# Optimization experiments

Measured on AMD Instinct MI355X. Metric: run time of the kernel, lower is better.

## Reference

```python
import jax, jax.numpy as jnp
import numpy as np

EPS = 1e-5

def _bn(x, g, b):
    # BatchNorm1d in training mode: batch statistics over nodes
    m = jnp.mean(x, axis=0)
    v = jnp.var(x, axis=0)
    return g * (x - m) * jax.lax.rsqrt(v + EPS) + b

def _gconv(x, adj, W, b):
    # GraphConvolution: adj @ x @ W + b
    return adj @ (x @ W) + b

def _gsage(x, adj, W, b):
    # GraphSAGE layer: relu(adj @ x @ W + b)
    return jax.nn.relu(adj @ (x @ W) + b)

def setup_inputs() -> dict:
    key = jax.random.key(0)
    ks = jax.random.split(key, 20)
    N = 8192
    x = jax.random.normal(ks[0], (N, 18), dtype=jnp.float32)
    adj = jax.random.uniform(ks[1], (N, N), dtype=jnp.float32)
    s = 0.1
    p = {
        'W1': jax.random.normal(ks[2], (18, 16)) * s, 'b1': jnp.zeros((16,)),
        'W2': jax.random.normal(ks[3], (16, 16)) * s, 'b2': jnp.zeros((16,)),
        'We1': jax.random.normal(ks[4], (16, 8)) * s, 'be1': jnp.zeros((8,)),
        'Wp1': jax.random.normal(ks[5], (16, 20)) * s, 'bp1': jnp.zeros((20,)),
        'W3': jax.random.normal(ks[6], (8, 8)) * s, 'b3': jnp.zeros((8,)),
        'We2': jax.random.normal(ks[7], (8, 8)) * s, 'be2': jnp.zeros((8,)),
        'g1': jnp.ones((16,)), 'bt1': jnp.zeros((16,)),
        'g2': jnp.ones((16,)), 'bt2': jnp.zeros((16,)),
        'g3': jnp.ones((8,)), 'bt3': jnp.zeros((8,)),
    }
    p = {k: v.astype(jnp.float32) for k, v in p.items()}
    return {'x': x, 'adj': adj, **p}

def reference(x, adj, W1, b1, W2, b2, We1, be1, Wp1, bp1, W3, b3, We2, be2,
              g1, bt1, g2, bt2, g3, bt3):
    h = _bn(_gsage(x, adj, W1, b1), g1, bt1)          # [N,16]
    h = _bn(_gsage(h, adj, W2, b2), g2, bt2)          # [N,16]
    # DiffPool(16, 20, 8)
    z = _gconv(h, adj, We1, be1)                      # [N,8]
    s_l = jax.nn.softmax(_gconv(h, adj, Wp1, bp1), axis=1)  # [N,20]
    h = s_l.T @ z                                     # [20,8]
    a = s_l.T @ adj @ s_l                             # [20,20]
    h = _bn(_gsage(h, a, W3, b3), g3, bt3)            # [20,8]
    # DiffPool(8, 1, 8, is_final=True): s = ones -> column sum
    z = _gconv(h, a, We2, be2)                        # [20,8]
    return jnp.sum(z, axis=0, keepdims=True)          # [1,8]
```

## Files before the change

### kernel.cpp

```cpp
#include <hip/hip_runtime.h>
#include <cstddef>

#define NROWS 8192
constexpr float BN_EPS = 1e-5f;

typedef __attribute__((ext_vector_type(8))) short bf16x8;
typedef __attribute__((ext_vector_type(4))) float f32x4;
typedef __attribute__((ext_vector_type(2))) float f32x2;
typedef __attribute__((ext_vector_type(4))) unsigned int u32x4;

__device__ __forceinline__ unsigned short bf16u(float f) {
    unsigned u = __float_as_uint(f);
    u += 0x7FFFu + ((u >> 16) & 1u);
    return (unsigned short)(u >> 16);
}
__device__ __forceinline__ unsigned bf16pk(float x, float y) {
    return (unsigned)bf16u(x) | ((unsigned)bf16u(y) << 16);
}

constexpr size_t OFF_P   = 0;
constexpr size_t OFF_YP  = OFF_P   + (size_t)16 * NROWS * 32;
constexpr size_t OFF_SLP = OFF_YP  + (size_t)NROWS * 32 / 2;
constexpr size_t OFF_U   = OFF_SLP + (size_t)NROWS * 32 / 2;
constexpr size_t OFF_SL  = OFF_U   + (size_t)NROWS * 16;
constexpr size_t OFF_ST1 = OFF_SL  + (size_t)NROWS * 20;
constexpr size_t OFF_ST2 = OFF_ST1 + 32;
constexpr size_t OFF_HSM = OFF_ST2 + 32;
constexpr size_t OFF_AG  = OFF_HSM + 160;
constexpr size_t OFF_CTR = OFF_AG  + 400;
constexpr int    NSMALL  = 32 + 32 + 160 + 400 + 2;
constexpr size_t OFF_END_SMALL = OFF_CTR + 2;
constexpr size_t OFF_ADJB = (OFF_END_SMALL + 15) & ~(size_t)15;
constexpr size_t NEED_FULL_BYTES = (OFF_ADJB + (size_t)NROWS * NROWS / 2) * 4;


__global__ __launch_bounds__(256)
void k_conv_spmm(const float* __restrict__ adjf, unsigned short* __restrict__ adjp,
                 const unsigned short* __restrict__ ypu, float* __restrict__ P)
{
    __shared__ unsigned short lds[16384];
    const int bid = blockIdx.x;
    const int rb = bid & 63, kc = bid >> 6;
    const int t = threadIdx.x, lane = t & 63, wv = t >> 6;
    const int row0 = rb * 128 + wv * 32;
    const int s_q = lane >> 4;
    const int khi = (lane >> 2) & 3;
    const int el2 = (lane & 3) * 2;
    const bf16x8* ap = (const bf16x8*)lds;
    const bf16x8* yp = (const bf16x8*)ypu;
    const size_t blockbase = (size_t)(kc * 64 + rb) * 8192;

    f32x4 acc0 = (f32x4){0.f,0.f,0.f,0.f}, acc1 = (f32x4){0.f,0.f,0.f,0.f};

    for (int q = 0; q < 4; ++q) {
        const int kbase = kc * 512 + q * 128;
        __syncthreads();
#pragma unroll 8
        for (int rr = 0; rr < 32; ++rr) {
            const f32x2 v = *(const f32x2*)(adjf + (size_t)(row0 + rr) * NROWS + kbase + lane * 2);
            const int m = rr >> 4, rA = rr & 15;
            int u = ((wv * 4 + s_q) * 2 + m) * 64 + rA + 16 * khi;
            u ^= ((u >> 4) & 3) ^ (((u >> 7) & 1) << 2);
            *(unsigned*)&lds[u * 8 + el2] = bf16pk(v.x, v.y);
        }
        __syncthreads();
#pragma unroll
        for (int i = 0; i < 8; ++i) {
            const int flat = i * 256 + t;
            const int phys = flat ^ ((flat >> 4) & 3) ^ (((flat >> 7) & 1) << 2);
            const u32x4 d = *(const u32x4*)&lds[phys * 8];
            const int wvd = flat >> 9;
            const size_t gu = blockbase + (size_t)wvd * 2048 + (size_t)q * 512 + (flat & 511);
            *(u32x4*)(adjp + gu * 8) = d;
        }
#pragma unroll
        for (int sq = 0; sq < 4; ++sq) {
            int L0 = ((wv * 4 + sq) * 2 + 0) * 64 + lane;
            int L1 = L0 + 64;
            L0 ^= ((L0 >> 4) & 3) ^ (((L0 >> 7) & 1) << 2);
            L1 ^= ((L1 >> 4) & 3) ^ (((L1 >> 7) & 1) << 2);
            const bf16x8 a0 = ap[L0];
            const bf16x8 a1 = ap[L1];
            const bf16x8 b0 = yp[((size_t)(kc * 16 + q * 4 + sq)) * 64 + lane];
            acc0 = __builtin_amdgcn_mfma_f32_16x16x32_bf16(a0, b0, acc0, 0, 0, 0);
            acc1 = __builtin_amdgcn_mfma_f32_16x16x32_bf16(a1, b0, acc1, 0, 0, 0);
        }
    }

    float* Pk = P + ((size_t)kc * NROWS + row0) * 16;
    const int drow = (lane >> 4) * 4;
    const int dcol = lane & 15;
#pragma unroll
    for (int r = 0; r < 4; ++r) {
        Pk[(size_t)(drow + r) * 16 + dcol]      = acc0[r];
        Pk[(size_t)(16 + drow + r) * 16 + dcol] = acc1[r];
    }
}

template<int NT, int CO>
__global__ __launch_bounds__(256)
void k_spmm_p(const unsigned short* __restrict__ adjp,
              const unsigned short* __restrict__ ypu, float* __restrict__ P)
{
    constexpr int CP = NT * 16;
    const int rb   = blockIdx.x & 63;
    const int kc2  = blockIdx.x >> 6;
    const int lane = threadIdx.x & 63;
    const int wv   = threadIdx.x >> 6;
    const int row0 = rb * 128 + wv * 32;
    const bf16x8* ap = (const bf16x8*)adjp;
    const bf16x8* yp = (const bf16x8*)ypu;
    const size_t wbase0 = ((size_t)((kc2 * 2 + 0) * 64 + rb) * 4 + wv) * 2048;
    const size_t wbase1 = ((size_t)((kc2 * 2 + 1) * 64 + rb) * 4 + wv) * 2048;

    f32x4 acc[2][NT];
#pragma unroll
    for (int m = 0; m < 2; ++m)
#pragma unroll
        for (int n = 0; n < NT; ++n) acc[m][n] = (f32x4){0.f, 0.f, 0.f, 0.f};

    auto LA = [&](int m, int s) -> bf16x8 {
        const size_t wb = (s < 16) ? wbase0 : wbase1;
        return ap[wb + (size_t)(s & 15) * 128 + m * 64 + lane];
    };
    auto LB = [&](int n, int s) -> bf16x8 {
        return yp[((size_t)((kc2 * 32 + s) * NT + n)) * 64 + lane];
    };

    bf16x8 a0 = LA(0, 0), a1 = LA(1, 0);
    bf16x8 b0 = LB(0, 0), b1;
    if constexpr (NT == 2) b1 = LB(1, 0);

#pragma unroll
    for (int s = 0; s < 32; ++s) {
        bf16x8 na0, na1, nb0, nb1;
        if (s < 31) {
            na0 = LA(0, s + 1); na1 = LA(1, s + 1);
            nb0 = LB(0, s + 1);
            if constexpr (NT == 2) nb1 = LB(1, s + 1);
        }
        acc[0][0] = __builtin_amdgcn_mfma_f32_16x16x32_bf16(a0, b0, acc[0][0], 0, 0, 0);
        acc[1][0] = __builtin_amdgcn_mfma_f32_16x16x32_bf16(a1, b0, acc[1][0], 0, 0, 0);
        if constexpr (NT == 2) {
            acc[0][1] = __builtin_amdgcn_mfma_f32_16x16x32_bf16(a0, b1, acc[0][1], 0, 0, 0);
            acc[1][1] = __builtin_amdgcn_mfma_f32_16x16x32_bf16(a1, b1, acc[1][1], 0, 0, 0);
        }
        if (s < 31) { a0 = na0; a1 = na1; b0 = nb0; if constexpr (NT == 2) b1 = nb1; }
    }

    float* Pk = P + ((size_t)kc2 * NROWS + row0) * CP;
    const int drow = (lane >> 4) * 4;
    const int dcol = lane & 15;
#pragma unroll
    for (int m = 0; m < 2; ++m)
#pragma unroll
        for (int n = 0; n < NT; ++n)
            if (n * 16 + 0 < CO)
#pragma unroll
                for (int r = 0; r < 4; ++r)
                    if (n * 16 + dcol < CO)
                        Pk[(size_t)(m * 16 + drow + r) * CP + n * 16 + dcol] = acc[m][n][r];
}

template<int NT, int CO>
__global__ __launch_bounds__(256)
void k_spmm_f32(const float* __restrict__ adjf,
                const unsigned short* __restrict__ ypu, float* __restrict__ P)
{
    constexpr int CP = NT * 16;
    const int rb   = blockIdx.x & 63;
    const int kc   = blockIdx.x >> 6;
    const int lane = threadIdx.x & 63;
    const int wv   = threadIdx.x >> 6;
    const int row0 = rb * 128 + wv * 32;
    const int k0   = kc * 512;
    const int rA   = lane & 15;
    const int kA   = (lane >> 4) * 8;
    const bf16x8* yp = (const bf16x8*)ypu;

    f32x4 acc[2][NT];
#pragma unroll
    for (int m = 0; m < 2; ++m)
#pragma unroll
        for (int n = 0; n < NT; ++n) acc[m][n] = (f32x4){0.f, 0.f, 0.f, 0.f};

    const size_t offA0 = (size_t)(row0 + rA) * NROWS + k0 + kA;
    const size_t offA1 = offA0 + (size_t)16 * NROWS;

    auto LA = [&](int m, int s) -> bf16x8 {
        const size_t o = (m ? offA1 : offA0) + (size_t)s * 32;
        const f32x4 u = *(const f32x4*)(adjf + o);
        const f32x4 v = *(const f32x4*)(adjf + o + 4);
        bf16x8 tt;
        tt[0] = (short)bf16u(u.x); tt[1] = (short)bf16u(u.y);
        tt[2] = (short)bf16u(u.z); tt[3] = (short)bf16u(u.w);
        tt[4] = (short)bf16u(v.x); tt[5] = (short)bf16u(v.y);
        tt[6] = (short)bf16u(v.z); tt[7] = (short)bf16u(v.w);
        return tt;
    };
    auto LB = [&](int n, int s) -> bf16x8 {
        return yp[((size_t)((kc * 16 + s) * NT + n)) * 64 + lane];
    };

    bf16x8 a0 = LA(0, 0), a1 = LA(1, 0);
    bf16x8 b0 = LB(0, 0), b1;
    if constexpr (NT == 2) b1 = LB(1, 0);

#pragma unroll
    for (int s = 0; s < 16; ++s) {
        bf16x8 na0, na1, nb0, nb1;
        if (s < 15) {
            na0 = LA(0, s + 1); na1 = LA(1, s + 1);
            nb0 = LB(0, s + 1);
            if constexpr (NT == 2) nb1 = LB(1, s + 1);
        }
        acc[0][0] = __builtin_amdgcn_mfma_f32_16x16x32_bf16(a0, b0, acc[0][0], 0, 0, 0);
        acc[1][0] = __builtin_amdgcn_mfma_f32_16x16x32_bf16(a1, b0, acc[1][0], 0, 0, 0);
        if constexpr (NT == 2) {
            acc[0][1] = __builtin_amdgcn_mfma_f32_16x16x32_bf16(a0, b1, acc[0][1], 0, 0, 0);
            acc[1][1] = __builtin_amdgcn_mfma_f32_16x16x32_bf16(a1, b1, acc[1][1], 0, 0, 0);
        }
        if (s < 15) { a0 = na0; a1 = na1; b0 = nb0; if constexpr (NT == 2) b1 = nb1; }
    }

    float* Pk = P + ((size_t)kc * NROWS + row0) * CP;
    const int drow = (lane >> 4) * 4;
    const int dcol = lane & 15;
#pragma unroll
    for (int m = 0; m < 2; ++m)
#pragma unroll
        for (int n = 0; n < NT; ++n)
            if (n * 16 + 0 < CO)
#pragma unroll
                for (int r = 0; r < 4; ++r)
                    if (n * 16 + dcol < CO)
                        Pk[(size_t)(m * 16 + drow + r) * CP + n * 16 + dcol] = acc[m][n][r];
}

__global__ __launch_bounds__(256)
void k_y1_pack(const float* __restrict__ x, const float* __restrict__ W1,
               unsigned short* __restrict__ yp, float* __restrict__ zsmall)
{
    if (blockIdx.x == 0) {
        for (int i = threadIdx.x; i < NSMALL; i += 256) zsmall[i] = 0.f;
    }
    const int j = blockIdx.x * 256 + threadIdx.x;
    float xr[18];
#pragma unroll
    for (int d = 0; d < 18; ++d) xr[d] = x[j * 18 + d];
    const int kb = j >> 5, lhi = ((j & 31) >> 3) << 4, idx = j & 7;
#pragma unroll
    for (int c = 0; c < 16; ++c) {
        float a = 0.f;
#pragma unroll
        for (int d = 0; d < 18; ++d) a = fmaf(xr[d], W1[d * 16 + c], a);
        yp[((size_t)kb * 64 + (lhi | c)) * 8 + idx] = bf16u(a);
    }
}

template<int KCN, int COA, int COB, int NTO>
__global__ __launch_bounds__(256)
void k_red_bn(const float* __restrict__ P, const float* __restrict__ bias,
              const float* __restrict__ g, const float* __restrict__ bt,
              const float* __restrict__ Wa, const float* __restrict__ Wb,
              unsigned short* __restrict__ yp, float* __restrict__ stats,
              unsigned int* __restrict__ ctr)
{
    const int t = threadIdx.x, col = t & 15, rg = t >> 4;
    const int rbase = blockIdx.x * 128;
    float u[8];
    float s = 0.f, ss = 0.f;
#pragma unroll
    for (int i = 0; i < 8; ++i) {
        const int r = rbase + rg + i * 16;
        float v = bias[col];
#pragma unroll
        for (int kc = 0; kc < KCN; ++kc)
            v += P[((size_t)kc * NROWS + r) * 16 + col];
        v = fmaxf(v, 0.f);
        u[i] = v; s += v; ss += v * v;
    }
    __shared__ float ls[16][17], lss[16][17];
    __shared__ float hb[128][17];
    __shared__ float scb[16], shb[16];
    ls[rg][col] = s; lss[rg][col] = ss;
    __syncthreads();
    if (t < 16) {
        float a = 0.f, b = 0.f;
        for (int gg = 0; gg < 16; ++gg) { a += ls[gg][t]; b += lss[gg][t]; }
        atomicAdd(&stats[t], a);
        atomicAdd(&stats[16 + t], b);
    }
    __syncthreads();
    if (t == 0) {
        __threadfence();
        atomicAdd(ctr, 1u);
        while (__hip_atomic_load(ctr, __ATOMIC_RELAXED, __HIP_MEMORY_SCOPE_AGENT) < 64u) {}
        __threadfence();
    }
    __syncthreads();
    if (t < 16) {
        const float sm  = atomicAdd(&stats[t], 0.f);
        const float sq  = atomicAdd(&stats[16 + t], 0.f);
        const float m   = sm * (1.f / NROWS);
        const float var = sq * (1.f / NROWS) - m * m;
        const float sc  = g[t] * rsqrtf(var + BN_EPS);
        scb[t] = sc; shb[t] = bt[t] - m * sc;
    }
    __syncthreads();
#pragma unroll
    for (int i = 0; i < 8; ++i)
        hb[rg + i * 16][col] = fmaf(u[i], scb[col], shb[col]);
    __syncthreads();
    constexpr int CO = COA + COB;
    const int lrow = t >> 1;
    const int jrow = rbase + lrow;
    const int kb = jrow >> 5, lhi = ((jrow & 31) >> 3) << 4, idx = jrow & 7;
    auto slot = [&](int c) -> size_t {
        return ((size_t)(kb * NTO + (c >> 4)) * 64 + (lhi | (c & 15))) * 8 + idx;
    };
    float h[16];
#pragma unroll
    for (int k = 0; k < 16; ++k) h[k] = hb[lrow][k];
    const int c0 = (t & 1) * ((NTO * 16) / 2);
#pragma unroll
    for (int cc = 0; cc < (NTO * 16) / 2; ++cc) {
        const int c = c0 + cc;
        float a = 0.f;
        if (c < COA) {
#pragma unroll
            for (int k = 0; k < 16; ++k) a = fmaf(h[k], Wa[k * COA + c], a);
        } else if (c < CO) {
#pragma unroll
            for (int k = 0; k < 16; ++k) a = fmaf(h[k], Wb[k * COB + (c - COA)], a);
        }
        yp[slot(c)] = (c < CO) ? bf16u(a) : (unsigned short)0;
    }
}

template<int KCN>
__global__ __launch_bounds__(256)
void k_red_fin3(const float* __restrict__ P, const float* __restrict__ be1,
                const float* __restrict__ bp1, float* __restrict__ sl,
                unsigned short* __restrict__ slp, float* __restrict__ hsm)
{
    __shared__ float szl[256 * 8];
    __shared__ float ssl[256 * 20];
    const int t = threadIdx.x;
    const int row = blockIdx.x * 256 + t;

    float s3[28];
#pragma unroll
    for (int c = 0; c < 28; ++c) s3[c] = 0.f;
#pragma unroll
    for (int kc = 0; kc < KCN; ++kc) {
        const float* pr = &P[((size_t)kc * NROWS + row) * 32];
#pragma unroll
        for (int q = 0; q < 7; ++q) {
            const f32x4 v = *(const f32x4*)(pr + q * 4);
            s3[q * 4 + 0] += v.x; s3[q * 4 + 1] += v.y;
            s3[q * 4 + 2] += v.z; s3[q * 4 + 3] += v.w;
        }
    }
#pragma unroll
    for (int k = 0; k < 8; ++k) szl[t * 8 + k] = s3[k] + be1[k];

    float s[20];
    float mx = -1e30f;
#pragma unroll
    for (int k = 0; k < 20; ++k) {
        s[k] = s3[8 + k] + bp1[k];
        mx = fmaxf(mx, s[k]);
    }
    float se = 0.f;
#pragma unroll
    for (int k = 0; k < 20; ++k) { s[k] = expf(s[k] - mx); se += s[k]; }
    const float inv = 1.f / se;
    const int kb = row >> 5, lhi = ((row & 31) >> 3) << 4, idx = row & 7;
    auto slot = [&](int c) -> size_t {
        return ((size_t)(kb * 2 + (c >> 4)) * 64 + (lhi | (c & 15))) * 8 + idx;
    };
#pragma unroll
    for (int k = 0; k < 20; ++k) {
        s[k] *= inv;
        sl[(size_t)row * 20 + k] = s[k];
        ssl[t * 20 + k] = s[k];
        slp[slot(k)] = bf16u(s[k]);
    }
#pragma unroll
    for (int c = 20; c < 32; ++c) slp[slot(c)] = 0;
    __syncthreads();
    if (t < 160) {
        const int p = t >> 3, q = t & 7;
        float a = 0.f;
        for (int r = 0; r < 256; ++r) a = fmaf(ssl[r * 20 + p], szl[r * 8 + q], a);
        atomicAdd(&hsm[t], a);
    }
}

template<int KCN>
__global__ __launch_bounds__(256)
void k_red_fin4(const float* __restrict__ P, const float* __restrict__ sl,
                float* __restrict__ a_g)
{
    __shared__ float stt[256 * 20];
    __shared__ float ssl[256 * 20];
    const int t = threadIdx.x;
    const int row = blockIdx.x * 256 + t;

    float t4[20];
#pragma unroll
    for (int c = 0; c < 20; ++c) t4[c] = 0.f;
#pragma unroll
    for (int kc = 0; kc < KCN; ++kc) {
        const float* pr = &P[((size_t)kc * NROWS + row) * 32];
#pragma unroll
        for (int q = 0; q < 5; ++q) {
            const f32x4 v = *(const f32x4*)(pr + q * 4);
            t4[q * 4 + 0] += v.x; t4[q * 4 + 1] += v.y;
            t4[q * 4 + 2] += v.z; t4[q * 4 + 3] += v.w;
        }
    }
#pragma unroll
    for (int c = 0; c < 20; ++c) {
        stt[t * 20 + c] = t4[c];
        ssl[t * 20 + c] = sl[(size_t)row * 20 + c];
    }
    __syncthreads();
    for (int pair = t; pair < 400; pair += 256) {
        const int p = pair / 20, q = pair % 20;
        float a = 0.f;
        for (int r = 0; r < 256; ++r) a = fmaf(ssl[r * 20 + p], stt[r * 20 + q], a);
        atomicAdd(&a_g[pair], a);
    }
}

__global__ __launch_bounds__(256)
void k_final(const float* __restrict__ hsm, const float* __restrict__ a_g,
             const float* __restrict__ W3, const float* __restrict__ b3,
             const float* __restrict__ g3, const float* __restrict__ bt3,
             const float* __restrict__ We2, const float* __restrict__ be2,
             float* __restrict__ out)
{
    __shared__ float m1[160], qb[160], hb[160], sc[8], sh[8];
    const int t = threadIdx.x;
    const int p = t >> 3, k = t & 7;
    if (t < 160) {
        float a = 0.f;
        for (int j = 0; j < 8; ++j) a = fmaf(hsm[p * 8 + j], W3[j * 8 + k], a);
        m1[t] = a;
    }
    __syncthreads();
    if (t < 160) {
        float a = b3[k];
        for (int j = 0; j < 20; ++j) a = fmaf(a_g[p * 20 + j], m1[j * 8 + k], a);
        qb[t] = fmaxf(a, 0.f);
    }
    __syncthreads();
    if (t < 8) {
        float m = 0.f, v = 0.f;
        for (int r = 0; r < 20; ++r) { float q = qb[r * 8 + t]; m += q; v += q * q; }
        m *= (1.f / 20.f); v = v * (1.f / 20.f) - m * m;
        const float s = g3[t] * rsqrtf(v + BN_EPS);
        sc[t] = s; sh[t] = bt3[t] - m * s;
    }
    __syncthreads();
    if (t < 160) hb[t] = fmaf(qb[t], sc[k], sh[k]);
    __syncthreads();
    if (t < 160) {
        float a = 0.f;
        for (int j = 0; j < 8; ++j) a = fmaf(hb[p * 8 + j], We2[j * 8 + k], a);
        m1[t] = a;
    }
    __syncthreads();
    if (t < 160) {
        float a = be2[k];
        for (int j = 0; j < 20; ++j) a = fmaf(a_g[p * 20 + j], m1[j * 8 + k], a);
        qb[t] = a;
    }
    __syncthreads();
    if (t < 8) {
        float a = 0.f;
        for (int r = 0; r < 20; ++r) a += qb[r * 8 + t];
        out[t] = a;
    }
}

extern "C" void kernel_launch(void* const* d_in, const int* in_sizes, int n_in,
                              void* d_out, int out_size, void* d_ws, size_t ws_size,
                              hipStream_t stream)
{
    const float* x   = (const float*)d_in[0];
    const float* adj = (const float*)d_in[1];
    const float* W1  = (const float*)d_in[2];
    const float* b1  = (const float*)d_in[3];
    const float* W2  = (const float*)d_in[4];
    const float* b2  = (const float*)d_in[5];
    const float* We1 = (const float*)d_in[6];
    const float* be1 = (const float*)d_in[7];
    const float* Wp1 = (const float*)d_in[8];
    const float* bp1 = (const float*)d_in[9];
    const float* W3  = (const float*)d_in[10];
    const float* b3  = (const float*)d_in[11];
    const float* We2 = (const float*)d_in[12];
    const float* be2 = (const float*)d_in[13];
    const float* g1  = (const float*)d_in[14];
    const float* bt1 = (const float*)d_in[15];
    const float* g2  = (const float*)d_in[16];
    const float* bt2 = (const float*)d_in[17];
    const float* g3  = (const float*)d_in[18];
    const float* bt3 = (const float*)d_in[19];

    float* ws = (float*)d_ws;
    float* P  = ws + OFF_P;
    unsigned short* YP   = (unsigned short*)(ws + OFF_YP);
    unsigned short* SLP  = (unsigned short*)(ws + OFF_SLP);
    float* SL  = ws + OFF_SL;
    float* ST1 = ws + OFF_ST1;
    float* ST2 = ws + OFF_ST2;
    float* HSM = ws + OFF_HSM;
    float* AG  = ws + OFF_AG;
    unsigned int* CTR = (unsigned int*)(ws + OFF_CTR);
    unsigned short* ADJP = (unsigned short*)(ws + OFF_ADJB);
    float* out = (float*)d_out;

    const bool FULL = ws_size >= NEED_FULL_BYTES;
    const dim3 blk(256);

    k_y1_pack<<<32, blk, 0, stream>>>(x, W1, YP, ST1);
    if (FULL) {
        k_conv_spmm<<<1024, blk, 0, stream>>>(adj, ADJP, YP, P);
        k_red_bn<16, 16, 0, 1><<<64, blk, 0, stream>>>(P, b1, g1, bt1, W2, nullptr, YP, ST1, CTR);

        k_spmm_p<1, 16><<<512, blk, 0, stream>>>(ADJP, YP, P);
        k_red_bn<8, 8, 20, 2><<<64, blk, 0, stream>>>(P, b2, g2, bt2, We1, Wp1, YP, ST2, CTR + 1);

        k_spmm_p<2, 28><<<512, blk, 0, stream>>>(ADJP, YP, P);
        k_red_fin3<8><<<32, blk, 0, stream>>>(P, be1, bp1, SL, SLP, HSM);

        k_spmm_p<2, 20><<<512, blk, 0, stream>>>(ADJP, SLP, P);
        k_red_fin4<8><<<32, blk, 0, stream>>>(P, SL, AG);
    } else {
        k_spmm_f32<1, 16><<<1024, blk, 0, stream>>>(adj, YP, P);
        k_red_bn<16, 16, 0, 1><<<64, blk, 0, stream>>>(P, b1, g1, bt1, W2, nullptr, YP, ST1, CTR);

        k_spmm_f32<1, 16><<<1024, blk, 0, stream>>>(adj, YP, P);
        k_red_bn<16, 8, 20, 2><<<64, blk, 0, stream>>>(P, b2, g2, bt2, We1, Wp1, YP, ST2, CTR + 1);

        k_spmm_f32<2, 28><<<1024, blk, 0, stream>>>(adj, YP, P);
        k_red_fin3<16><<<32, blk, 0, stream>>>(P, be1, bp1, SL, SLP, HSM);

        k_spmm_f32<2, 20><<<1024, blk, 0, stream>>>(adj, SLP, P);
        k_red_fin4<16><<<32, blk, 0, stream>>>(P, SL, AG);
    }

    k_final<<<1, blk, 0, stream>>>(HSM, AG, W3, b3, g3, bt3, We2, be2, out);
}
```

Before: 197.8 us.

## Fuse SpMM passes with their reductions using last-block grid sync

Merges each bf16 SpMM pass over the packed adjacency with the reduction/BN/softmax kernel that followed it. Every block bumps an atomic counter after writing partials, and the first 32 or 64 blocks spin until all 512 have arrived before doing the reduction. This removes three kernel launches and the gaps between them. In exchange the spinning blocks hold resources and rely on every block being co-resident or already finished, which risks deadlock. The change also adds launch-bounds occupancy hints and a larger unroll in the conversion kernel.

```diff
diff --git a/kernel.cpp b/kernel.cpp
--- a/kernel.cpp
+++ b/kernel.cpp
@@ -28,13 +28,13 @@
 constexpr size_t OFF_HSM = OFF_ST2 + 32;
 constexpr size_t OFF_AG  = OFF_HSM + 160;
 constexpr size_t OFF_CTR = OFF_AG  + 400;
-constexpr int    NSMALL  = 32 + 32 + 160 + 400 + 2;
-constexpr size_t OFF_END_SMALL = OFF_CTR + 2;
+constexpr int    NSMALL  = 32 + 32 + 160 + 400 + 8;
+constexpr size_t OFF_END_SMALL = OFF_CTR + 8;
 constexpr size_t OFF_ADJB = (OFF_END_SMALL + 15) & ~(size_t)15;
 constexpr size_t NEED_FULL_BYTES = (OFF_ADJB + (size_t)NROWS * NROWS / 2) * 4;
 
 
-__global__ __launch_bounds__(256)
+__global__ __launch_bounds__(256, 4)
 void k_conv_spmm(const float* __restrict__ adjf, unsigned short* __restrict__ adjp,
                  const unsigned short* __restrict__ ypu, float* __restrict__ P)
 {
@@ -55,7 +55,7 @@
     for (int q = 0; q < 4; ++q) {
         const int kbase = kc * 512 + q * 128;
         __syncthreads();
-#pragma unroll 8
+#pragma unroll 16
         for (int rr = 0; rr < 32; ++rr) {
             const f32x2 v = *(const f32x2*)(adjf + (size_t)(row0 + rr) * NROWS + kbase + lane * 2);
             const int m = rr >> 4, rA = rr & 15;
@@ -97,12 +97,137 @@
     }
 }
 
-template<int NT, int CO>
-__global__ __launch_bounds__(256)
-void k_spmm_p(const unsigned short* __restrict__ adjp,
-              const unsigned short* __restrict__ ypu, float* __restrict__ P)
-{
-    constexpr int CP = NT * 16;
+__global__ __launch_bounds__(256, 4)
+void k_spmm_bn(const unsigned short* __restrict__ adjp, unsigned short* yp_io,
+               float* __restrict__ P, const float* __restrict__ bias,
+               const float* __restrict__ g, const float* __restrict__ bt,
+               const float* __restrict__ Wa, const float* __restrict__ Wb,
+               float* __restrict__ stats, unsigned int* __restrict__ ctrs)
+{
+    const int rb   = blockIdx.x & 63;
+    const int kc2  = blockIdx.x >> 6;
+    const int lane = threadIdx.x & 63;
+    const int wv   = threadIdx.x >> 6;
+    const int row0 = rb * 128 + wv * 32;
+    const bf16x8* ap = (const bf16x8*)adjp;
+    const bf16x8* yp = (const bf16x8*)yp_io;
+    const size_t wbase0 = ((size_t)((kc2 * 2 + 0) * 64 + rb) * 4 + wv) * 2048;
+    const size_t wbase1 = ((size_t)((kc2 * 2 + 1) * 64 + rb) * 4 + wv) * 2048;
+
+    f32x4 acc0 = (f32x4){0.f,0.f,0.f,0.f}, acc1 = (f32x4){0.f,0.f,0.f,0.f};
+    auto LA = [&](int m, int s) -> bf16x8 {
+        const size_t wb = (s < 16) ? wbase0 : wbase1;
+        return ap[wb + (size_t)(s & 15) * 128 + m * 64 + lane];
+    };
+    auto LB = [&](int s) -> bf16x8 {
+        return yp[((size_t)(kc2 * 32 + s)) * 64 + lane];
+    };
+    bf16x8 a0 = LA(0, 0), a1 = LA(1, 0), b0 = LB(0);
+#pragma unroll
+    for (int s = 0; s < 32; ++s) {
+        bf16x8 na0, na1, nb0;
+        if (s < 31) { na0 = LA(0, s + 1); na1 = LA(1, s + 1); nb0 = LB(s + 1); }
+        acc0 = __builtin_amdgcn_mfma_f32_16x16x32_bf16(a0, b0, acc0, 0, 0, 0);
+        acc1 = __builtin_amdgcn_mfma_f32_16x16x32_bf16(a1, b0, acc1, 0, 0, 0);
+        if (s < 31) { a0 = na0; a1 = na1; b0 = nb0; }
+    }
+    {
+        float* Pk = P + ((size_t)kc2 * NROWS + row0) * 16;
+        const int drow = (lane >> 4) * 4, dcol = lane & 15;
+#pragma unroll
+        for (int r = 0; r < 4; ++r) {
+            Pk[(size_t)(drow + r) * 16 + dcol]      = acc0[r];
+            Pk[(size_t)(16 + drow + r) * 16 + dcol] = acc1[r];
+        }
+    }
+    __threadfence();
+    __syncthreads();
+    if (threadIdx.x == 0) atomicAdd(&ctrs[0], 1u);
+    if (blockIdx.x >= 64) return;
+    if (threadIdx.x == 0) {
+        while (__hip_atomic_load(&ctrs[0], __ATOMIC_RELAXED, __HIP_MEMORY_SCOPE_AGENT) < 512u) {}
+        __threadfence();
+    }
+    __syncthreads();
+
+    const int t = threadIdx.x, col = t & 15, rg = t >> 4;
+    const int rbase = blockIdx.x * 128;
+    float u[8];
+    float s = 0.f, ss = 0.f;
+#pragma unroll
+    for (int i = 0; i < 8; ++i) {
+        const int r = rbase + rg + i * 16;
+        float v = bias[col];
+#pragma unroll
+        for (int kc = 0; kc < 8; ++kc)
+            v += P[((size_t)kc * NROWS + r) * 16 + col];
+        v = fmaxf(v, 0.f);
+        u[i] = v; s += v; ss += v * v;
+    }
+    __shared__ float ls[16][17], lss[16][17];
+    __shared__ float hb[128][17];
+    __shared__ float scb[16], shb[16];
+    ls[rg][col] = s; lss[rg][col] = ss;
+    __syncthreads();
+    if (t < 16) {
+        float a = 0.f, b = 0.f;
+        for (int gg = 0; gg < 16; ++gg) { a += ls[gg][t]; b += lss[gg][t]; }
+        atomicAdd(&stats[t], a);
+        atomicAdd(&stats[16 + t], b);
+    }
+    __syncthreads();
+    if (t == 0) {
+        __threadfence();
+        atomicAdd(&ctrs[1], 1u);
+        while (__hip_atomic_load(&ctrs[1], __ATOMIC_RELAXED, __HIP_MEMORY_SCOPE_AGENT) < 64u) {}
+        __threadfence();
+    }
+    __syncthreads();
+    if (t < 16) {
+        const float sm  = atomicAdd(&stats[t], 0.f);
+        const float sq  = atomicAdd(&stats[16 + t], 0.f);
+        const float m   = sm * (1.f / NROWS);
+        const float var = sq * (1.f / NROWS) - m * m;
+        const float sc  = g[t] * rsqrtf(var + BN_EPS);
+        scb[t] = sc; shb[t] = bt[t] - m * sc;
+    }
+    __syncthreads();
+#pragma unroll
+    for (int i = 0; i < 8; ++i)
+        hb[rg + i * 16][col] = fmaf(u[i], scb[col], shb[col]);
+    __syncthreads();
+    const int lrow = t >> 1;
+    const int jrow = rbase + lrow;
+    const int kb = jrow >> 5, lhi = ((jrow & 31) >> 3) << 4, idx = jrow & 7;
+    auto slot = [&](int c) -> size_t {
+        return ((size_t)(kb * 2 + (c >> 4)) * 64 + (lhi | (c & 15))) * 8 + idx;
+    };
+    float h[16];
+#pragma unroll
+    for (int k = 0; k < 16; ++k) h[k] = hb[lrow][k];
+    const int c0 = (t & 1) * 16;
+#pragma unroll
+    for (int cc = 0; cc < 16; ++cc) {
+        const int c = c0 + cc;
+        float a = 0.f;
+        if (c < 8) {
+#pragma unroll
+            for (int k = 0; k < 16; ++k) a = fmaf(h[k], Wa[k * 8 + c], a);
+        } else if (c < 28) {
+#pragma unroll
+            for (int k = 0; k < 16; ++k) a = fmaf(h[k], Wb[k * 20 + (c - 8)], a);
+        }
+        yp_io[slot(c)] = (c < 28) ? bf16u(a) : (unsigned short)0;
+    }
+}
+
+__global__ __launch_bounds__(256, 4)
+void k_spmm_fin3(const unsigned short* __restrict__ adjp,
+                 const unsigned short* __restrict__ ypu, float* __restrict__ P,
+                 const float* __restrict__ be1, const float* __restrict__ bp1,
+                 float* __restrict__ sl, unsigned short* __restrict__ slp,
+                 float* __restrict__ hsm, unsigned int* __restrict__ ctr)
+{
     const int rb   = blockIdx.x & 63;
     const int kc2  = blockIdx.x >> 6;
     const int lane = threadIdx.x & 63;
@@ -113,53 +238,193 @@
     const size_t wbase0 = ((size_t)((kc2 * 2 + 0) * 64 + rb) * 4 + wv) * 2048;
     const size_t wbase1 = ((size_t)((kc2 * 2 + 1) * 64 + rb) * 4 + wv) * 2048;
 
-    f32x4 acc[2][NT];
+    f32x4 acc[2][2];
 #pragma unroll
     for (int m = 0; m < 2; ++m)
 #pragma unroll
-        for (int n = 0; n < NT; ++n) acc[m][n] = (f32x4){0.f, 0.f, 0.f, 0.f};
-
+        for (int n = 0; n < 2; ++n) acc[m][n] = (f32x4){0.f, 0.f, 0.f, 0.f};
     auto LA = [&](int m, int s) -> bf16x8 {
         const size_t wb = (s < 16) ? wbase0 : wbase1;
         return ap[wb + (size_t)(s & 15) * 128 + m * 64 + lane];
     };
     auto LB = [&](int n, int s) -> bf16x8 {
-        return yp[((size_t)((kc2 * 32 + s) * NT + n)) * 64 + lane];
-    };
-
-    bf16x8 a0 = LA(0, 0), a1 = LA(1, 0);
-    bf16x8 b0 = LB(0, 0), b1;
-    if constexpr (NT == 2) b1 = LB(1, 0);
-
+        return yp[((size_t)((kc2 * 32 + s) * 2 + n)) * 64 + lane];
+    };
+    bf16x8 a0 = LA(0, 0), a1 = LA(1, 0), b0 = LB(0, 0), b1 = LB(1, 0);
 #pragma unroll
     for (int s = 0; s < 32; ++s) {
         bf16x8 na0, na1, nb0, nb1;
-        if (s < 31) {
-            na0 = LA(0, s + 1); na1 = LA(1, s + 1);
-            nb0 = LB(0, s + 1);
-            if constexpr (NT == 2) nb1 = LB(1, s + 1);
-        }
+        if (s < 31) { na0 = LA(0, s+1); na1 = LA(1, s+1); nb0 = LB(0, s+1); nb1 = LB(1, s+1); }
         acc[0][0] = __builtin_amdgcn_mfma_f32_16x16x32_bf16(a0, b0, acc[0][0], 0, 0, 0);
         acc[1][0] = __builtin_amdgcn_mfma_f32_16x16x32_bf16(a1, b0, acc[1][0], 0, 0, 0);
-        if constexpr (NT == 2) {
-            acc[0][1] = __builtin_amdgcn_mfma_f32_16x16x32_bf16(a0, b1, acc[0][1], 0, 0, 0);
-            acc[1][1] = __builtin_amdgcn_mfma_f32_16x16x32_bf16(a1, b1, acc[1][1], 0, 0, 0);
-        }
-        if (s < 31) { a0 = na0; a1 = na1; b0 = nb0; if constexpr (NT == 2) b1 = nb1; }
-    }
-
-    float* Pk = P + ((size_t)kc2 * NROWS + row0) * CP;
-    const int drow = (lane >> 4) * 4;
-    const int dcol = lane & 15;
+        acc[0][1] = __builtin_amdgcn_mfma_f32_16x16x32_bf16(a0, b1, acc[0][1], 0, 0, 0);
+        acc[1][1] = __builtin_amdgcn_mfma_f32_16x16x32_bf16(a1, b1, acc[1][1], 0, 0, 0);
+        if (s < 31) { a0 = na0; a1 = na1; b0 = nb0; b1 = nb1; }
+    }
+    {
+        float* Pk = P + ((size_t)kc2 * NROWS + row0) * 32;
+        const int drow = (lane >> 4) * 4, dcol = lane & 15;
+#pragma unroll
+        for (int m = 0; m < 2; ++m)
+#pragma unroll
+            for (int n = 0; n < 2; ++n)
+#pragma unroll
+                for (int r = 0; r < 4; ++r)
+                    if (n * 16 + dcol < 28)
+                        Pk[(size_t)(m * 16 + drow + r) * 32 + n * 16 + dcol] = acc[m][n][r];
+    }
+    __threadfence();
+    __syncthreads();
+    if (threadIdx.x == 0) atomicAdd(ctr, 1u);
+    if (blockIdx.x >= 32) return;
+    if (threadIdx.x == 0) {
+        while (__hip_atomic_load(ctr, __ATOMIC_RELAXED, __HIP_MEMORY_SCOPE_AGENT) < 512u) {}
+        __threadfence();
+    }
+    __syncthreads();
+
+    __shared__ float szl[256 * 8];
+    __shared__ float ssl[256 * 20];
+    const int t = threadIdx.x;
+    const int row = blockIdx.x * 256 + t;
+    float s3[28];
+#pragma unroll
+    for (int c = 0; c < 28; ++c) s3[c] = 0.f;
+#pragma unroll
+    for (int kc = 0; kc < 8; ++kc) {
+        const float* pr = &P[((size_t)kc * NROWS + row) * 32];
+#pragma unroll
+        for (int q = 0; q < 7; ++q) {
+            const f32x4 v = *(const f32x4*)(pr + q * 4);
+            s3[q * 4 + 0] += v.x; s3[q * 4 + 1] += v.y;
+            s3[q * 4 + 2] += v.z; s3[q * 4 + 3] += v.w;
+        }
+    }
+#pragma unroll
+    for (int k = 0; k < 8; ++k) szl[t * 8 + k] = s3[k] + be1[k];
+    float s[20];
+    float mx = -1e30f;
+#pragma unroll
+    for (int k = 0; k < 20; ++k) {
+        s[k] = s3[8 + k] + bp1[k];
+        mx = fmaxf(mx, s[k]);
+    }
+    float se = 0.f;
+#pragma unroll
+    for (int k = 0; k < 20; ++k) { s[k] = expf(s[k] - mx); se += s[k]; }
+    const float inv = 1.f / se;
+    const int kb = row >> 5, lhi = ((row & 31) >> 3) << 4, idx = row & 7;
+    auto slot = [&](int c) -> size_t {
+        return ((size_t)(kb * 2 + (c >> 4)) * 64 + (lhi | (c & 15))) * 8 + idx;
+    };
+#pragma unroll
+    for (int k = 0; k < 20; ++k) {
+        s[k] *= inv;
+        sl[(size_t)row * 20 + k] = s[k];
+        ssl[t * 20 + k] = s[k];
+        slp[slot(k)] = bf16u(s[k]);
+    }
+#pragma unroll
+    for (int c = 20; c < 32; ++c) slp[slot(c)] = 0;
+    __syncthreads();
+    if (t < 160) {
+        const int p = t >> 3, q = t & 7;
+        float a = 0.f;
+        for (int r = 0; r < 256; ++r) a = fmaf(ssl[r * 20 + p], szl[r * 8 + q], a);
+        atomicAdd(&hsm[t], a);
+    }
+}
+
+__global__ __launch_bounds__(256, 4)
+void k_spmm_fin4(const unsigned short* __restrict__ adjp,
+                 const unsigned short* __restrict__ slpu, float* __restrict__ P,
+                 const float* __restrict__ sl, float* __restrict__ a_g,
+                 unsigned int* __restrict__ ctr)
+{
+    const int rb   = blockIdx.x & 63;
+    const int kc2  = blockIdx.x >> 6;
+    const int lane = threadIdx.x & 63;
+    const int wv   = threadIdx.x >> 6;
+    const int row0 = rb * 128 + wv * 32;
+    const bf16x8* ap = (const bf16x8*)adjp;
+    const bf16x8* yp = (const bf16x8*)slpu;
+    const size_t wbase0 = ((size_t)((kc2 * 2 + 0) * 64 + rb) * 4 + wv) * 2048;
+    const size_t wbase1 = ((size_t)((kc2 * 2 + 1) * 64 + rb) * 4 + wv) * 2048;
+
+    f32x4 acc[2][2];
 #pragma unroll
     for (int m = 0; m < 2; ++m)
 #pragma unroll
-        for (int n = 0; n < NT; ++n)
-            if (n * 16 + 0 < CO)
+        for (int n = 0; n < 2; ++n) acc[m][n] = (f32x4){0.f, 0.f, 0.f, 0.f};
+    auto LA = [&](int m, int s) -> bf16x8 {
+        const size_t wb = (s < 16) ? wbase0 : wbase1;
+        return ap[wb + (size_t)(s & 15) * 128 + m * 64 + lane];
+    };
+    auto LB = [&](int n, int s) -> bf16x8 {
+        return yp[((size_t)((kc2 * 32 + s) * 2 + n)) * 64 + lane];
+    };
+    bf16x8 a0 = LA(0, 0), a1 = LA(1, 0), b0 = LB(0, 0), b1 = LB(1, 0);
+#pragma unroll
+    for (int s = 0; s < 32; ++s) {
+        bf16x8 na0, na1, nb0, nb1;
+        if (s < 31) { na0 = LA(0, s+1); na1 = LA(1, s+1); nb0 = LB(0, s+1); nb1 = LB(1, s+1); }
+        acc[0][0] = __builtin_amdgcn_mfma_f32_16x16x32_bf16(a0, b0, acc[0][0], 0, 0, 0);
+        acc[1][0] = __builtin_amdgcn_mfma_f32_16x16x32_bf16(a1, b0, acc[1][0], 0, 0, 0);
+        acc[0][1] = __builtin_amdgcn_mfma_f32_16x16x32_bf16(a0, b1, acc[0][1], 0, 0, 0);
+        acc[1][1] = __builtin_amdgcn_mfma_f32_16x16x32_bf16(a1, b1, acc[1][1], 0, 0, 0);
+        if (s < 31) { a0 = na0; a1 = na1; b0 = nb0; b1 = nb1; }
+    }
+    {
+        float* Pk = P + ((size_t)kc2 * NROWS + row0) * 32;
+        const int drow = (lane >> 4) * 4, dcol = lane & 15;
+#pragma unroll
+        for (int m = 0; m < 2; ++m)
+#pragma unroll
+            for (int n = 0; n < 2; ++n)
 #pragma unroll
                 for (int r = 0; r < 4; ++r)
-                    if (n * 16 + dcol < CO)
-                        Pk[(size_t)(m * 16 + drow + r) * CP + n * 16 + dcol] = acc[m][n][r];
+                    if (n * 16 + dcol < 20)
+                        Pk[(size_t)(m * 16 + drow + r) * 32 + n * 16 + dcol] = acc[m][n][r];
+    }
+    __threadfence();
+    __syncthreads();
+    if (threadIdx.x == 0) atomicAdd(ctr, 1u);
+    if (blockIdx.x >= 32) return;
+    if (threadIdx.x == 0) {
+        while (__hip_atomic_load(ctr, __ATOMIC_RELAXED, __HIP_MEMORY_SCOPE_AGENT) < 512u) {}
+        __threadfence();
+    }
+    __syncthreads();
+
+    __shared__ float stt[256 * 20];
+    __shared__ float ssl[256 * 20];
+    const int t = threadIdx.x;
+    const int row = blockIdx.x * 256 + t;
+    float t4[20];
+#pragma unroll
+    for (int c = 0; c < 20; ++c) t4[c] = 0.f;
+#pragma unroll
+    for (int kc = 0; kc < 8; ++kc) {
+        const float* pr = &P[((size_t)kc * NROWS + row) * 32];
+#pragma unroll
+        for (int q = 0; q < 5; ++q) {
+            const f32x4 v = *(const f32x4*)(pr + q * 4);
+            t4[q * 4 + 0] += v.x; t4[q * 4 + 1] += v.y;
+            t4[q * 4 + 2] += v.z; t4[q * 4 + 3] += v.w;
+        }
+    }
+#pragma unroll
+    for (int c = 0; c < 20; ++c) {
+        stt[t * 20 + c] = t4[c];
+        ssl[t * 20 + c] = sl[(size_t)row * 20 + c];
+    }
+    __syncthreads();
+    for (int pair = t; pair < 400; pair += 256) {
+        const int p = pair / 20, q = pair % 20;
+        float a = 0.f;
+        for (int r = 0; r < 256; ++r) a = fmaf(ssl[r * 20 + p], stt[r * 20 + q], a);
+        atomicAdd(&a_g[pair], a);
+    }
 }
 
 template<int NT, int CO>
@@ -348,7 +613,6 @@
     __shared__ float ssl[256 * 20];
     const int t = threadIdx.x;
     const int row = blockIdx.x * 256 + t;
-
     float s3[28];
 #pragma unroll
     for (int c = 0; c < 28; ++c) s3[c] = 0.f;
@@ -364,7 +628,6 @@
     }
 #pragma unroll
     for (int k = 0; k < 8; ++k) szl[t * 8 + k] = s3[k] + be1[k];
-
     float s[20];
     float mx = -1e30f;
 #pragma unroll
@@ -407,7 +670,6 @@
     __shared__ float ssl[256 * 20];
     const int t = threadIdx.x;
     const int row = blockIdx.x * 256 + t;
-
     float t4[20];
 #pragma unroll
     for (int c = 0; c < 20; ++c) t4[c] = 0.f;
@@ -532,14 +794,11 @@
         k_conv_spmm<<<1024, blk, 0, stream>>>(adj, ADJP, YP, P);
         k_red_bn<16, 16, 0, 1><<<64, blk, 0, stream>>>(P, b1, g1, bt1, W2, nullptr, YP, ST1, CTR);
 
-        k_spmm_p<1, 16><<<512, blk, 0, stream>>>(ADJP, YP, P);
-        k_red_bn<8, 8, 20, 2><<<64, blk, 0, stream>>>(P, b2, g2, bt2, We1, Wp1, YP, ST2, CTR + 1);
-
-        k_spmm_p<2, 28><<<512, blk, 0, stream>>>(ADJP, YP, P);
-        k_red_fin3<8><<<32, blk, 0, stream>>>(P, be1, bp1, SL, SLP, HSM);
-
-        k_spmm_p<2, 20><<<512, blk, 0, stream>>>(ADJP, SLP, P);
-        k_red_fin4<8><<<32, blk, 0, stream>>>(P, SL, AG);
+        k_spmm_bn<<<512, blk, 0, stream>>>(ADJP, YP, P, b2, g2, bt2, We1, Wp1, ST2, CTR + 1);
+
+        k_spmm_fin3<<<512, blk, 0, stream>>>(ADJP, YP, P, be1, bp1, SL, SLP, HSM, CTR + 3);
+
+        k_spmm_fin4<<<512, blk, 0, stream>>>(ADJP, SLP, P, SL, AG, CTR + 4);
     } else {
         k_spmm_f32<1, 16><<<1024, blk, 0, stream>>>(adj, YP, P);
         k_red_bn<16, 16, 0, 1><<<64, blk, 0, stream>>>(P, b1, g1, bt1, W2, nullptr, YP, ST1, CTR);
```

Result: slower. 401.6 us (+103.0%).
